# Optimization experiments

Hardware: AMD Instinct MI355X
Metric: run time of the kernel (lower is better)

Reference implementation:

```python
import jax, jax.numpy as jnp
import numpy as np

N_NODES = 100000
EPS = 1e-12  # F.normalize eps


def mean_aggregate(x, src, dst):
    # gather source features along edges, segment-mean into destinations
    msg = x[src]                                              # [E, D]
    summed = jax.ops.segment_sum(msg, dst, num_segments=N_NODES)  # [N, D]
    cnt = jax.ops.segment_sum(jnp.ones_like(dst, dtype=x.dtype), dst,
                              num_segments=N_NODES)           # [N]
    return summed / jnp.maximum(cnt, 1.0)[:, None]


def sage_conv(x, src, dst, W_l, b_l, W_r, normalize):
    agg = mean_aggregate(x, src, dst)
    out = agg @ W_l.T + b_l + x @ W_r.T  # lin_l(mean neigh) + lin_r(root)
    if normalize:
        norm = jnp.sqrt(jnp.sum(out * out, axis=-1, keepdims=True))
        out = out / jnp.maximum(norm, EPS)
    return out


def setup_inputs() -> dict:
    key = jax.random.key(0)
    ks = jax.random.split(key, 8)
    H, O = 128, 128
    s = 1.0 / np.sqrt(H)
    x = jax.random.normal(ks[0], (N_NODES, H), dtype=jnp.float32)
    edge_index = jax.random.randint(ks[1], (2, 1600000), 0, N_NODES, dtype=jnp.int64)
    return {
        "x": x,
        "edge_index": edge_index,
        "W1l": jax.random.uniform(ks[2], (H, H), jnp.float32, -s, s),
        "b1": jax.random.uniform(ks[3], (H,), jnp.float32, -s, s),
        "W1r": jax.random.uniform(ks[4], (H, H), jnp.float32, -s, s),
        "W2l": jax.random.uniform(ks[5], (O, H), jnp.float32, -s, s),
        "b2": jax.random.uniform(ks[6], (O,), jnp.float32, -s, s),
        "W2r": jax.random.uniform(ks[7], (O, H), jnp.float32, -s, s),
    }


def reference(x, edge_index, W1l, b1, W1r, W2l, b2, W2r):
    src, dst = edge_index[0], edge_index[1]
    h = sage_conv(x, src, dst, W1l, b1, W1r, normalize=True)
    h = jax.nn.relu(h)
    out = sage_conv(h, src, dst, W2l, b2, W2r, normalize=False)
    return out
```

## Files before the change

### kernel.cpp

```cpp
#include <hip/hip_runtime.h>
#include <hip/hip_bf16.h>
#include <hip/hip_fp16.h>

#define N_NODES 100000
#define DFEAT 128
#define SLAB 4096
#define BSHIFT 9
#define NBUCK 196

#define WS_CNT      0
#define WS_GH       100000
#define WS_PARTB    180000
#define WS_OFFS     200000
#define WS_ESRC     300608
#define WS_AGGH     1900608
#define WS_CASTH    8300608

typedef _Float16 half8 __attribute__((ext_vector_type(8)));
typedef _Float16 half2v __attribute__((ext_vector_type(2)));
typedef float floatx4 __attribute__((ext_vector_type(4)));

__global__ __launch_bounds__(256) void prep_kernel(const float* __restrict__ x,
                                                   __half* __restrict__ xh, int total4,
                                                   const int* __restrict__ dst,
                                                   int* __restrict__ gh,
                                                   int E, int bpart, int castblocks) {
    __shared__ int lh[NBUCK];
    int b = blockIdx.x;
    if (b < castblocks) {
        int i = b * 256 + threadIdx.x;
        if (i < total4) {
            float4 v = ((const float4*)x)[i];
            __half2 h01 = __floats2half2_rn(v.x, v.y);
            __half2 h23 = __floats2half2_rn(v.z, v.w);
            uint2 o;
            o.x = *(unsigned int*)&h01;
            o.y = *(unsigned int*)&h23;
            ((uint2*)xh)[i] = o;
        }
        return;
    }
    int bb = b - castblocks;
    for (int i = threadIdx.x; i < NBUCK; i += 256) lh[i] = 0;
    __syncthreads();
    int s0 = bb * SLAB, s1 = min(E, s0 + SLAB);
    for (int i = s0 + threadIdx.x; i < s1; i += 256)
        atomicAdd(&lh[dst[i] >> BSHIFT], 1);
    __syncthreads();
    for (int i = threadIdx.x; i < NBUCK; i += 256) gh[i * bpart + bb] = lh[i];
}

__global__ void scan1_kernel(int* __restrict__ gh, int* __restrict__ partial, int m) {
    __shared__ int s[256];
    int i = blockIdx.x * 256 + threadIdx.x;
    int v = (i < m) ? gh[i] : 0;
    s[threadIdx.x] = v;
    __syncthreads();
    for (int d = 1; d < 256; d <<= 1) {
        int t = (threadIdx.x >= d) ? s[threadIdx.x - d] : 0;
        __syncthreads();
        s[threadIdx.x] += t;
        __syncthreads();
    }
    int incl = s[threadIdx.x];
    if (i < m) gh[i] = incl - v;
    if (threadIdx.x == 255) partial[blockIdx.x] = incl;
}

__global__ void scan2_kernel(int* __restrict__ partial, int nb) {
    __shared__ int s[512];
    int t = threadIdx.x;
    int v = (t < nb) ? partial[t] : 0;
    s[t] = v;
    __syncthreads();
    for (int d = 1; d < 512; d <<= 1) {
        int u = (t >= d) ? s[t - d] : 0;
        __syncthreads();
        s[t] += u;
        __syncthreads();
    }
    if (t < nb) partial[t] = s[t] - v;
}

__global__ void scan3_kernel(int* __restrict__ gh, const int* __restrict__ partial, int m) {
    int i = blockIdx.x * 256 + threadIdx.x;
    if (i < m) gh[i] += partial[blockIdx.x];
}

__global__ __launch_bounds__(256) void phase2_kernel(const int* __restrict__ src,
                                                     const int* __restrict__ dst,
                                                     const int* __restrict__ gbase,
                                                     int2* __restrict__ pairs,
                                                     int E, int bpart) {
    __shared__ int lbase[NBUCK];
    __shared__ int lcur[NBUCK];
    __shared__ int lgb[NBUCK];
    __shared__ int sc[256];
    __shared__ int2 lp[SLAB];
    int b = blockIdx.x;
    int t = threadIdx.x;
    for (int i = t; i < NBUCK; i += 256) lbase[i] = 0;
    __syncthreads();
    int s0 = b * SLAB, s1 = min(E, s0 + SLAB);
    for (int i = s0 + t; i < s1; i += 256)
        atomicAdd(&lbase[dst[i] >> BSHIFT], 1);
    __syncthreads();
    int v = (t < NBUCK) ? lbase[t] : 0;
    sc[t] = v;
    __syncthreads();
    for (int d = 1; d < 256; d <<= 1) {
        int u = (t >= d) ? sc[t - d] : 0;
        __syncthreads();
        sc[t] += u;
        __syncthreads();
    }
    if (t < NBUCK) {
        int excl = sc[t] - v;
        lbase[t] = excl;
        lcur[t] = excl;
        lgb[t] = gbase[t * bpart + b];
    }
    __syncthreads();
    for (int i = s0 + t; i < s1; i += 256) {
        int d = dst[i];
        int s = src[i];
        int bk = d >> BSHIFT;
        int pos = atomicAdd(&lcur[bk], 1);
        lp[pos] = make_int2(s, d);
    }
    __syncthreads();
    int m = s1 - s0;
    for (int i = t; i < m; i += 256) {
        int2 p = lp[i];
        int bk = p.y >> BSHIFT;
        pairs[lgb[bk] + (i - lbase[bk])] = p;
    }
}

__global__ __launch_bounds__(512) void phase3_kernel(const int2* __restrict__ pairs,
                                                     const int* __restrict__ gbase,
                                                     int* __restrict__ cnt,
                                                     int* __restrict__ offs,
                                                     int* __restrict__ esrc,
                                                     int E, int bpart, int n) {
    __shared__ int lcnt[512];
    __shared__ int sc[512];
    __shared__ int lexcl[512];
    int g = blockIdx.x;
    int node0 = g << BSHIFT;
    int t = threadIdx.x;
    lcnt[t] = 0;
    __syncthreads();
    int S = gbase[g * bpart];
    int Eg = (g == NBUCK - 1) ? E : gbase[(g + 1) * bpart];
    for (int i = S + t; i < Eg; i += 512)
        atomicAdd(&lcnt[pairs[i].y - node0], 1);
    __syncthreads();
    int v = lcnt[t];
    sc[t] = v;
    __syncthreads();
    for (int d = 1; d < 512; d <<= 1) {
        int u = (t >= d) ? sc[t - d] : 0;
        __syncthreads();
        sc[t] += u;
        __syncthreads();
    }
    int excl = sc[t] - v;
    lexcl[t] = excl;
    int nd = node0 + t;
    if (nd < n) {
        cnt[nd] = v;
        offs[nd] = S + excl;
    }
    __syncthreads();
    for (int i = S + t; i < Eg; i += 512) {
        int2 p = pairs[i];
        int pos = atomicAdd(&lexcl[p.y - node0], 1);
        esrc[S + pos] = p.x;
    }
}

__global__ void aggregate_kernel(const __half* __restrict__ feat, const int* __restrict__ esrc,
                                 const int* __restrict__ offs, const int* __restrict__ cnt,
                                 __half* __restrict__ agg, int n) {
    int wid = (blockIdx.x * blockDim.x + threadIdx.x) >> 6;
    int lane = threadIdx.x & 63;
    if (wid >= n) return;
    int beg = offs[wid];
    int deg = cnt[wid];
    int half_id = lane >> 5;
    int colbase = (lane & 31) * 4;
    half2v s01 = (half2v)(_Float16)0;
    half2v s23 = (half2v)(_Float16)0;

    for (int base = 0; base < deg; base += 64) {
        int m = min(64, deg - base);
        int idx = (lane < m) ? esrc[beg + base + lane] : 0;
#pragma unroll 8
        for (int j = 0; j < m; j += 2) {
            int jj = j + half_id;
            bool valid = jj < m;
            int s = __shfl(idx, valid ? jj : (m - 1));
            uint2 raw = *(const uint2*)(feat + (size_t)s * DFEAT + colbase);
            if (!valid) { raw.x = 0u; raw.y = 0u; }
            s01 += *(half2v*)&raw.x;
            s23 += *(half2v*)&raw.y;
        }
    }
    float a0 = (float)s01.x, a1 = (float)s01.y;
    float a2 = (float)s23.x, a3 = (float)s23.y;
    a0 += __shfl_xor(a0, 32);
    a1 += __shfl_xor(a1, 32);
    a2 += __shfl_xor(a2, 32);
    a3 += __shfl_xor(a3, 32);

    if (lane < 32) {
        float scale = 1.0f / fmaxf((float)deg, 1.0f);
        __half2 h01 = __floats2half2_rn(a0 * scale, a1 * scale);
        __half2 h23 = __floats2half2_rn(a2 * scale, a3 * scale);
        uint2 o;
        o.x = *(unsigned int*)&h01;
        o.y = *(unsigned int*)&h23;
        *(uint2*)(agg + (size_t)wid * DFEAT + colbase) = o;
    }
}

template <bool NORM_RELU>
__global__ __launch_bounds__(256) void gemm_mfma_kernel(
    const __half* __restrict__ A1_, const __half* __restrict__ A2_,
    const float* __restrict__ Wl, const float* __restrict__ Wr,
    const float* __restrict__ bias, float* __restrict__ out32,
    __half* __restrict__ out16, int n) {
    __shared__ __align__(16) _Float16 lw[128 * 136];

    const _Float16* A1 = (const _Float16*)A1_;
    const _Float16* A2 = (const _Float16*)A2_;

    const int lane = threadIdx.x & 63;
    const int w = threadIdx.x >> 6;
    const int quad = lane >> 4;
    const int l15 = lane & 15;
    const int i0 = blockIdx.x * 128 + w * 32;

    floatx4 acc[2][8];
#pragma unroll
    for (int nt = 0; nt < 2; nt++)
#pragma unroll
        for (int ft = 0; ft < 8; ft++)
            acc[nt][ft] = (floatx4){0.f, 0.f, 0.f, 0.f};

    int r0 = i0 + l15;      if (r0 >= n) r0 = n - 1;
    int r1 = i0 + 16 + l15; if (r1 >= n) r1 = n - 1;
    const int kq = quad * 8;

    for (int half = 0; half < 2; half++) {
        const float* __restrict__ W = half ? Wr : Wl;
        const _Float16* __restrict__ A = half ? A2 : A1;
        if (half) __syncthreads();
        {
            int t = threadIdx.x;
            int row = t >> 1;
            int cb = (t & 1) * 64;
            const float4* sp = (const float4*)(W + row * DFEAT + cb);
            unsigned int* dp = (unsigned int*)&lw[row * 136 + cb];
#pragma unroll
            for (int q = 0; q < 16; q++) {
                float4 v = sp[q];
                __half2 h01 = __floats2half2_rn(v.x, v.y);
                __half2 h23 = __floats2half2_rn(v.z, v.w);
                dp[q * 2] = *(unsigned int*)&h01;
                dp[q * 2 + 1] = *(unsigned int*)&h23;
            }
        }
        __syncthreads();
#pragma unroll
        for (int kc = 0; kc < DFEAT; kc += 32) {
            half8 b0 = *(const half8*)(A + (size_t)r0 * DFEAT + kc + kq);
            half8 b1 = *(const half8*)(A + (size_t)r1 * DFEAT + kc + kq);
#pragma unroll
            for (int ft = 0; ft < 8; ft++) {
                half8 a = *(const half8*)&lw[(ft * 16 + l15) * 136 + kc + kq];
                acc[0][ft] = __builtin_amdgcn_mfma_f32_16x16x32_f16(a, b0, acc[0][ft], 0, 0, 0);
                acc[1][ft] = __builtin_amdgcn_mfma_f32_16x16x32_f16(a, b1, acc[1][ft], 0, 0, 0);
            }
        }
    }

#pragma unroll
    for (int nt = 0; nt < 2; nt++) {
        int node = i0 + nt * 16 + l15;
        float v[8][4];
#pragma unroll
        for (int ft = 0; ft < 8; ft++) {
            const float4 bq = *(const float4*)(bias + ft * 16 + quad * 4);
            v[ft][0] = acc[nt][ft][0] + bq.x;
            v[ft][1] = acc[nt][ft][1] + bq.y;
            v[ft][2] = acc[nt][ft][2] + bq.z;
            v[ft][3] = acc[nt][ft][3] + bq.w;
        }
        if (NORM_RELU) {
            float ss = 0.f;
#pragma unroll
            for (int ft = 0; ft < 8; ft++)
#pragma unroll
                for (int r = 0; r < 4; r++) ss = fmaf(v[ft][r], v[ft][r], ss);
            ss += __shfl_xor(ss, 16);
            ss += __shfl_xor(ss, 32);
            float inv = 1.0f / fmaxf(sqrtf(ss), 1e-12f);
#pragma unroll
            for (int ft = 0; ft < 8; ft++)
#pragma unroll
                for (int r = 0; r < 4; r++) v[ft][r] = fmaxf(v[ft][r] * inv, 0.0f);
        }
        if (node < n) {
            if (NORM_RELU) {
                __half* op = (__half*)out16 + (size_t)node * DFEAT + quad * 4;
#pragma unroll
                for (int ft = 0; ft < 8; ft++) {
                    __half2 h01 = __floats2half2_rn(v[ft][0], v[ft][1]);
                    __half2 h23 = __floats2half2_rn(v[ft][2], v[ft][3]);
                    uint2 o;
                    o.x = *(unsigned int*)&h01;
                    o.y = *(unsigned int*)&h23;
                    *(uint2*)(op + ft * 16) = o;
                }
            } else {
                float* op = out32 + (size_t)node * DFEAT + quad * 4;
#pragma unroll
                for (int ft = 0; ft < 8; ft++)
                    *(float4*)(op + ft * 16) = make_float4(v[ft][0], v[ft][1], v[ft][2], v[ft][3]);
            }
        }
    }
}

extern "C" void kernel_launch(void* const* d_in, const int* in_sizes, int n_in,
                              void* d_out, int out_size, void* d_ws, size_t ws_size,
                              hipStream_t stream) {
    const float* x = (const float*)d_in[0];
    const int* edge_index = (const int*)d_in[1];
    const float* W1l = (const float*)d_in[2];
    const float* b1 = (const float*)d_in[3];
    const float* W1r = (const float*)d_in[4];
    const float* W2l = (const float*)d_in[5];
    const float* b2 = (const float*)d_in[6];
    const float* W2r = (const float*)d_in[7];
    float* out = (float*)d_out;

    const int E = in_sizes[1] / 2;
    const int n = in_sizes[0] / DFEAT;

    int* ws = (int*)d_ws;
    int* cnt = ws + WS_CNT;
    int* gh = ws + WS_GH;
    int* partialB = ws + WS_PARTB;
    int* offs = ws + WS_OFFS;
    int* esrc = ws + WS_ESRC;
    int2* pairs = (int2*)(ws + WS_AGGH);
    __half* aggh = (__half*)(ws + WS_AGGH);
    __half* casth = (__half*)(ws + WS_CASTH);

    const int* src = edge_index;
    const int* dst = edge_index + E;

    const int bpart = (E + SLAB - 1) / SLAB;
    const int m = NBUCK * bpart;
    const int blocksB = (m + 255) / 256;
    const int total4 = n * DFEAT / 4;
    const int castblocks = (total4 + 255) / 256;

    prep_kernel<<<castblocks + bpart, 256, 0, stream>>>(x, casth, total4, dst, gh,
                                                        E, bpart, castblocks);
    scan1_kernel<<<blocksB, 256, 0, stream>>>(gh, partialB, m);
    scan2_kernel<<<1, 512, 0, stream>>>(partialB, blocksB);
    scan3_kernel<<<blocksB, 256, 0, stream>>>(gh, partialB, m);

    phase2_kernel<<<bpart, 256, 0, stream>>>(src, dst, gh, pairs, E, bpart);
    phase3_kernel<<<NBUCK, 512, 0, stream>>>(pairs, gh, cnt, offs, esrc, E, bpart, n);

    const int aggb = (n * 64 + 255) / 256;
    const int gemmb = (n + 127) / 128;

    aggregate_kernel<<<aggb, 256, 0, stream>>>(casth, esrc, offs, cnt, aggh, n);
    gemm_mfma_kernel<true><<<gemmb, 256, 0, stream>>>(aggh, casth, W1l, W1r, b1, nullptr, aggh, n);

    aggregate_kernel<<<aggb, 256, 0, stream>>>(aggh, esrc, offs, cnt, casth, n);
    gemm_mfma_kernel<false><<<gemmb, 256, 0, stream>>>(casth, aggh, W2l, W2r, b2, out, nullptr, n);
}
```

Baseline: 380.8 us.

## Fuse mean aggregation into MFMA GEMM layer kernel, gathering directly into fragments

Replaces the separate aggregate and GEMM kernels with one fused per-layer kernel. Each lane gathers neighbour rows for its two nodes straight into the B-operand half8 fragments, scales them by the inverse degree, and feeds them to MFMA. A zero row in the workspace serves as padding for neighbours past a node's degree. This removes the aggregated-feature round trip through global memory and two launches. In exchange, the gather now uses one row per lane across 16-node groups bounded by the maximum degree, which can leave lanes idle on degree imbalance. It also reduces gather parallelism per node compared with the wave-per-node scheme.

```diff
diff --git a/kernel.cpp b/kernel.cpp
--- a/kernel.cpp
+++ b/kernel.cpp
@@ -11,19 +11,20 @@
 #define WS_CNT      0
 #define WS_GH       100000
 #define WS_PARTB    180000
+#define WS_ZROW     180512
 #define WS_OFFS     200000
 #define WS_ESRC     300608
 #define WS_AGGH     1900608
 #define WS_CASTH    8300608
 
 typedef _Float16 half8 __attribute__((ext_vector_type(8)));
-typedef _Float16 half2v __attribute__((ext_vector_type(2)));
 typedef float floatx4 __attribute__((ext_vector_type(4)));
 
 __global__ __launch_bounds__(256) void prep_kernel(const float* __restrict__ x,
                                                    __half* __restrict__ xh, int total4,
                                                    const int* __restrict__ dst,
                                                    int* __restrict__ gh,
+                                                   uint2* __restrict__ zrow,
                                                    int E, int bpart, int castblocks) {
     __shared__ int lh[NBUCK];
     int b = blockIdx.x;
@@ -41,6 +42,7 @@
         return;
     }
     int bb = b - castblocks;
+    if (bb == 0 && threadIdx.x < 32) zrow[threadIdx.x] = make_uint2(0u, 0u);
     for (int i = threadIdx.x; i < NBUCK; i += 256) lh[i] = 0;
     __syncthreads();
     int s0 = bb * SLAB, s1 = min(E, s0 + SLAB);
@@ -180,61 +182,17 @@
     }
 }
 
-__global__ void aggregate_kernel(const __half* __restrict__ feat, const int* __restrict__ esrc,
-                                 const int* __restrict__ offs, const int* __restrict__ cnt,
-                                 __half* __restrict__ agg, int n) {
-    int wid = (blockIdx.x * blockDim.x + threadIdx.x) >> 6;
-    int lane = threadIdx.x & 63;
-    if (wid >= n) return;
-    int beg = offs[wid];
-    int deg = cnt[wid];
-    int half_id = lane >> 5;
-    int colbase = (lane & 31) * 4;
-    half2v s01 = (half2v)(_Float16)0;
-    half2v s23 = (half2v)(_Float16)0;
-
-    for (int base = 0; base < deg; base += 64) {
-        int m = min(64, deg - base);
-        int idx = (lane < m) ? esrc[beg + base + lane] : 0;
-#pragma unroll 8
-        for (int j = 0; j < m; j += 2) {
-            int jj = j + half_id;
-            bool valid = jj < m;
-            int s = __shfl(idx, valid ? jj : (m - 1));
-            uint2 raw = *(const uint2*)(feat + (size_t)s * DFEAT + colbase);
-            if (!valid) { raw.x = 0u; raw.y = 0u; }
-            s01 += *(half2v*)&raw.x;
-            s23 += *(half2v*)&raw.y;
-        }
-    }
-    float a0 = (float)s01.x, a1 = (float)s01.y;
-    float a2 = (float)s23.x, a3 = (float)s23.y;
-    a0 += __shfl_xor(a0, 32);
-    a1 += __shfl_xor(a1, 32);
-    a2 += __shfl_xor(a2, 32);
-    a3 += __shfl_xor(a3, 32);
-
-    if (lane < 32) {
-        float scale = 1.0f / fmaxf((float)deg, 1.0f);
-        __half2 h01 = __floats2half2_rn(a0 * scale, a1 * scale);
-        __half2 h23 = __floats2half2_rn(a2 * scale, a3 * scale);
-        uint2 o;
-        o.x = *(unsigned int*)&h01;
-        o.y = *(unsigned int*)&h23;
-        *(uint2*)(agg + (size_t)wid * DFEAT + colbase) = o;
-    }
-}
-
 template <bool NORM_RELU>
-__global__ __launch_bounds__(256) void gemm_mfma_kernel(
-    const __half* __restrict__ A1_, const __half* __restrict__ A2_,
+__global__ __launch_bounds__(256, 4) void fused_layer_kernel(
+    const __half* __restrict__ feat_, const int* __restrict__ esrc,
+    const int* __restrict__ offs, const int* __restrict__ cnt,
     const float* __restrict__ Wl, const float* __restrict__ Wr,
-    const float* __restrict__ bias, float* __restrict__ out32,
-    __half* __restrict__ out16, int n) {
+    const float* __restrict__ bias, const __half* __restrict__ zrow_,
+    float* __restrict__ out32, __half* __restrict__ out16, int n) {
     __shared__ __align__(16) _Float16 lw[128 * 136];
 
-    const _Float16* A1 = (const _Float16*)A1_;
-    const _Float16* A2 = (const _Float16*)A2_;
+    const _Float16* feat = (const _Float16*)feat_;
+    const _Float16* zrow = (const _Float16*)zrow_;
 
     const int lane = threadIdx.x & 63;
     const int w = threadIdx.x >> 6;
@@ -242,6 +200,75 @@
     const int l15 = lane & 15;
     const int i0 = blockIdx.x * 128 + w * 32;
 
+    {
+        int t = threadIdx.x;
+        int row = t >> 1;
+        int cb = (t & 1) * 64;
+        const float4* sp = (const float4*)(Wl + row * DFEAT + cb);
+        unsigned int* dp = (unsigned int*)&lw[row * 136 + cb];
+#pragma unroll
+        for (int q = 0; q < 16; q++) {
+            float4 v = sp[q];
+            __half2 h01 = __floats2half2_rn(v.x, v.y);
+            __half2 h23 = __floats2half2_rn(v.z, v.w);
+            dp[q * 2] = *(unsigned int*)&h01;
+            dp[q * 2 + 1] = *(unsigned int*)&h23;
+        }
+    }
+
+    int r0 = i0 + l15;      if (r0 >= n) r0 = n - 1;
+    int r1 = i0 + 16 + l15; if (r1 >= n) r1 = n - 1;
+    int deg0 = cnt[r0], off0 = offs[r0];
+    int deg1 = cnt[r1], off1 = offs[r1];
+    int md = max(deg0, deg1);
+    md = max(md, __shfl_xor(md, 1));
+    md = max(md, __shfl_xor(md, 2));
+    md = max(md, __shfl_xor(md, 4));
+    md = max(md, __shfl_xor(md, 8));
+
+    const _Float16* fq = feat + quad * 8;
+    const _Float16* zq = zrow + quad * 8;
+
+    half8 bf0[4], bf1[4];
+#pragma unroll
+    for (int k = 0; k < 4; k++) {
+        bf0[k] = (half8)(_Float16)0;
+        bf1[k] = (half8)(_Float16)0;
+    }
+
+    for (int j = 0; j < md; j++) {
+        int s0 = esrc[off0 + j];
+        int s1 = esrc[off1 + j];
+        const _Float16* p0 = (j < deg0) ? (fq + (size_t)s0 * DFEAT) : zq;
+        const _Float16* p1 = (j < deg1) ? (fq + (size_t)s1 * DFEAT) : zq;
+        half8 t00 = *(const half8*)(p0);
+        half8 t01 = *(const half8*)(p0 + 32);
+        half8 t02 = *(const half8*)(p0 + 64);
+        half8 t03 = *(const half8*)(p0 + 96);
+        half8 t10 = *(const half8*)(p1);
+        half8 t11 = *(const half8*)(p1 + 32);
+        half8 t12 = *(const half8*)(p1 + 64);
+        half8 t13 = *(const half8*)(p1 + 96);
+        bf0[0] += t00; bf0[1] += t01; bf0[2] += t02; bf0[3] += t03;
+        bf1[0] += t10; bf1[1] += t11; bf1[2] += t12; bf1[3] += t13;
+    }
+
+    float sc0 = 1.0f / fmaxf((float)deg0, 1.0f);
+    float sc1 = 1.0f / fmaxf((float)deg1, 1.0f);
+#pragma unroll
+    for (int k = 0; k < 4; k++) {
+        half8 a = bf0[k], b = bf1[k];
+#pragma unroll
+        for (int e = 0; e < 8; e++) {
+            a[e] = (_Float16)((float)a[e] * sc0);
+            b[e] = (_Float16)((float)b[e] * sc1);
+        }
+        bf0[k] = a;
+        bf1[k] = b;
+    }
+
+    __syncthreads();
+
     floatx4 acc[2][8];
 #pragma unroll
     for (int nt = 0; nt < 2; nt++)
@@ -249,40 +276,53 @@
         for (int ft = 0; ft < 8; ft++)
             acc[nt][ft] = (floatx4){0.f, 0.f, 0.f, 0.f};
 
-    int r0 = i0 + l15;      if (r0 >= n) r0 = n - 1;
-    int r1 = i0 + 16 + l15; if (r1 >= n) r1 = n - 1;
-    const int kq = quad * 8;
-
-    for (int half = 0; half < 2; half++) {
-        const float* __restrict__ W = half ? Wr : Wl;
-        const _Float16* __restrict__ A = half ? A2 : A1;
-        if (half) __syncthreads();
-        {
-            int t = threadIdx.x;
-            int row = t >> 1;
-            int cb = (t & 1) * 64;
-            const float4* sp = (const float4*)(W + row * DFEAT + cb);
-            unsigned int* dp = (unsigned int*)&lw[row * 136 + cb];
-#pragma unroll
-            for (int q = 0; q < 16; q++) {
-                float4 v = sp[q];
-                __half2 h01 = __floats2half2_rn(v.x, v.y);
-                __half2 h23 = __floats2half2_rn(v.z, v.w);
-                dp[q * 2] = *(unsigned int*)&h01;
-                dp[q * 2 + 1] = *(unsigned int*)&h23;
-            }
-        }
-        __syncthreads();
-#pragma unroll
-        for (int kc = 0; kc < DFEAT; kc += 32) {
-            half8 b0 = *(const half8*)(A + (size_t)r0 * DFEAT + kc + kq);
-            half8 b1 = *(const half8*)(A + (size_t)r1 * DFEAT + kc + kq);
-#pragma unroll
-            for (int ft = 0; ft < 8; ft++) {
-                half8 a = *(const half8*)&lw[(ft * 16 + l15) * 136 + kc + kq];
-                acc[0][ft] = __builtin_amdgcn_mfma_f32_16x16x32_f16(a, b0, acc[0][ft], 0, 0, 0);
-                acc[1][ft] = __builtin_amdgcn_mfma_f32_16x16x32_f16(a, b1, acc[1][ft], 0, 0, 0);
-            }
+#pragma unroll
+    for (int kci = 0; kci < 4; kci++) {
+#pragma unroll
+        for (int ft = 0; ft < 8; ft++) {
+            half8 a = *(const half8*)&lw[(ft * 16 + l15) * 136 + kci * 32 + quad * 8];
+            acc[0][ft] = __builtin_amdgcn_mfma_f32_16x16x32_f16(a, bf0[kci], acc[0][ft], 0, 0, 0);
+            acc[1][ft] = __builtin_amdgcn_mfma_f32_16x16x32_f16(a, bf1[kci], acc[1][ft], 0, 0, 0);
+        }
+    }
+
+    __syncthreads();
+
+    half8 xf0[4], xf1[4];
+    {
+        const _Float16* xr0 = feat + (size_t)r0 * DFEAT + quad * 8;
+        const _Float16* xr1 = feat + (size_t)r1 * DFEAT + quad * 8;
+#pragma unroll
+        for (int k = 0; k < 4; k++) {
+            xf0[k] = *(const half8*)(xr0 + k * 32);
+            xf1[k] = *(const half8*)(xr1 + k * 32);
+        }
+    }
+
+    {
+        int t = threadIdx.x;
+        int row = t >> 1;
+        int cb = (t & 1) * 64;
+        const float4* sp = (const float4*)(Wr + row * DFEAT + cb);
+        unsigned int* dp = (unsigned int*)&lw[row * 136 + cb];
+#pragma unroll
+        for (int q = 0; q < 16; q++) {
+            float4 v = sp[q];
+            __half2 h01 = __floats2half2_rn(v.x, v.y);
+            __half2 h23 = __floats2half2_rn(v.z, v.w);
+            dp[q * 2] = *(unsigned int*)&h01;
+            dp[q * 2 + 1] = *(unsigned int*)&h23;
+        }
+    }
+    __syncthreads();
+
+#pragma unroll
+    for (int kci = 0; kci < 4; kci++) {
+#pragma unroll
+        for (int ft = 0; ft < 8; ft++) {
+            half8 a = *(const half8*)&lw[(ft * 16 + l15) * 136 + kci * 32 + quad * 8];
+            acc[0][ft] = __builtin_amdgcn_mfma_f32_16x16x32_f16(a, xf0[kci], acc[0][ft], 0, 0, 0);
+            acc[1][ft] = __builtin_amdgcn_mfma_f32_16x16x32_f16(a, xf1[kci], acc[1][ft], 0, 0, 0);
         }
     }
 
@@ -359,6 +399,7 @@
     int2* pairs = (int2*)(ws + WS_AGGH);
     __half* aggh = (__half*)(ws + WS_AGGH);
     __half* casth = (__half*)(ws + WS_CASTH);
+    uint2* zrow = (uint2*)(ws + WS_ZROW);
 
     const int* src = edge_index;
     const int* dst = edge_index + E;
@@ -369,7 +410,7 @@
     const int total4 = n * DFEAT / 4;
     const int castblocks = (total4 + 255) / 256;
 
-    prep_kernel<<<castblocks + bpart, 256, 0, stream>>>(x, casth, total4, dst, gh,
+    prep_kernel<<<castblocks + bpart, 256, 0, stream>>>(x, casth, total4, dst, gh, zrow,
                                                         E, bpart, castblocks);
     scan1_kernel<<<blocksB, 256, 0, stream>>>(gh, partialB, m);
     scan2_kernel<<<1, 512, 0, stream>>>(partialB, blocksB);
@@ -378,12 +419,11 @@
     phase2_kernel<<<bpart, 256, 0, stream>>>(src, dst, gh, pairs, E, bpart);
     phase3_kernel<<<NBUCK, 512, 0, stream>>>(pairs, gh, cnt, offs, esrc, E, bpart, n);
 
-    const int aggb = (n * 64 + 255) / 256;
     const int gemmb = (n + 127) / 128;
 
-    aggregate_kernel<<<aggb, 256, 0, stream>>>(casth, esrc, offs, cnt, aggh, n);
-    gemm_mfma_kernel<true><<<gemmb, 256, 0, stream>>>(aggh, casth, W1l, W1r, b1, nullptr, aggh, n);
-
-    aggregate_kernel<<<aggb, 256, 0, stream>>>(aggh, esrc, offs, cnt, casth, n);
-    gemm_mfma_kernel<false><<<gemmb, 256, 0, stream>>>(casth, aggh, W2l, W2r, b2, out, nullptr, n);
-}
+    fused_layer_kernel<true><<<gemmb, 256, 0, stream>>>(
+        casth, esrc, offs, cnt, W1l, W1r, b1, (const __half*)zrow, nullptr, aggh, n);
+
+    fused_layer_kernel<false><<<gemmb, 256, 0, stream>>>(
+        aggh, esrc, offs, cnt, W2l, W2r, b2, (const __half*)zrow, out, nullptr, n);
+}
```

Measured after the change: 394.1 us. 1.04x slower.
